# Kernel tuning notes

Measured on AMD Instinct MI355X. Metric: run time of the kernel, lower is better.

The kernel has to match this reference:

```python
import jax, jax.numpy as jnp
import numpy as np

L, B, S, C, H, V = 12, 2, 1024, 768, 12, 50257
D = C // H
FF = 4 * C
SCALE = 1.0 / float(np.sqrt(D))


def setup_inputs() -> dict:
    key = jax.random.key(0)
    ks = jax.random.split(key, 10)
    s = 0.02  # GPT-2 init std
    return {
        "idx": jax.random.randint(ks[0], (B, S), 0, V),
        "targets": jax.random.randint(ks[1], (B, S), 0, V),
        "wte": jax.random.normal(ks[2], (V, C), jnp.float32) * s,
        "wpe": jax.random.normal(ks[3], (S, C), jnp.float32) * s,
        "ln1_w": jnp.ones((L, C), jnp.float32),
        "ln1_b": jnp.zeros((L, C), jnp.float32),
        "qkv_w": jax.random.normal(ks[4], (L, C, 3 * C), jnp.float32) * s,
        "qkv_b": jnp.zeros((L, 3 * C), jnp.float32),
        "proj_w": jax.random.normal(ks[5], (L, C, C), jnp.float32) * s,
        "proj_b": jnp.zeros((L, C), jnp.float32),
        "ln2_w": jnp.ones((L, C), jnp.float32),
        "ln2_b": jnp.zeros((L, C), jnp.float32),
        "fc_w": jax.random.normal(ks[6], (L, C, FF), jnp.float32) * s,
        "fc_b": jnp.zeros((L, FF), jnp.float32),
        "fc2_w": jax.random.normal(ks[7], (L, FF, C), jnp.float32) * s,
        "fc2_b": jnp.zeros((L, C), jnp.float32),
        "lnf_w": jnp.ones((C,), jnp.float32),
        "lnf_b": jnp.zeros((C,), jnp.float32),
    }


def _ln(x, w, b):
    m = jnp.mean(x, axis=-1, keepdims=True)
    v = jnp.mean(jnp.square(x - m), axis=-1, keepdims=True)
    return (x - m) * jax.lax.rsqrt(v + 1e-5) * w + b


def _gpt(wte, wpe, ln1_w, ln1_b, qkv_w, qkv_b, proj_w, proj_b,
         ln2_w, ln2_b, fc_w, fc_b, fc2_w, fc2_b, lnf_w, lnf_b, idx, targets):
    h = wte[idx] + wpe[jnp.arange(S)]  # [B,S,C]
    causal = jnp.tril(jnp.ones((S, S), bool))

    def block(h, p):
        l1w, l1b, qw, qb, pw, pb, l2w, l2b, fw, fb, gw, gb = p
        x = _ln(h, l1w, l1b)
        q, k, v = jnp.split(x @ qw + qb, 3, axis=-1)  # each [B,S,C]
        heads = lambda t: t.reshape(B, S, H, D).transpose(0, 2, 1, 3)  # [B,H,S,D]
        q, k, v = heads(q), heads(k), heads(v)
        scores = jnp.einsum('bhsd,bhtd->bhst', q, k) * SCALE
        scores = jnp.where(causal, scores, -jnp.inf)
        att = jax.nn.softmax(scores, axis=-1)
        o = jnp.einsum('bhst,bhtd->bhsd', att, v)
        o = o.transpose(0, 2, 1, 3).reshape(B, S, C)
        h = h + o @ pw + pb
        x = _ln(h, l2w, l2b)
        h = h + jax.nn.gelu(x @ fw + fb, approximate=True) @ gw + gb
        return h, None

    h, _ = jax.lax.scan(block, h, (ln1_w, ln1_b, qkv_w, qkv_b, proj_w, proj_b,
                                   ln2_w, ln2_b, fc_w, fc_b, fc2_w, fc2_b))
    logits = _ln(h, lnf_w, lnf_b) @ wte.T  # tied lm_head, [B,S,V]
    logp = jax.nn.log_softmax(logits, axis=-1)
    loss = -jnp.mean(jnp.take_along_axis(logp, targets[..., None], axis=-1))
    return logits, loss


def reference(idx, targets, wte, wpe, ln1_w, ln1_b, qkv_w, qkv_b, proj_w, proj_b,
              ln2_w, ln2_b, fc_w, fc_b, fc2_w, fc2_b, lnf_w, lnf_b):
    return _gpt(wte, wpe, ln1_w, ln1_b, qkv_w, qkv_b, proj_w, proj_b,
                ln2_w, ln2_b, fc_w, fc_b, fc2_w, fc2_b, lnf_w, lnf_b, idx, targets)
```

## Files before the change

### kernel.cpp

```cpp
#include <hip/hip_runtime.h>
#include <hip/hip_bf16.h>
#include <cstdint>
#include <cstddef>

constexpr int LNUM = 12;
constexpr int BB   = 2;
constexpr int SS   = 1024;
constexpr int CC   = 768;
constexpr int HH   = 12;
constexpr int DD   = 64;
constexpr int FFD  = 3072;
constexpr int VV   = 50257;
constexpr int VPAD = 50304;
constexpr int MM   = BB * SS;
constexpr int NBX  = VPAD / 128;

typedef unsigned short u16;
typedef short     s16x8 __attribute__((ext_vector_type(8)));
typedef float     f32x4 __attribute__((ext_vector_type(4)));
typedef u16       u16x4 __attribute__((ext_vector_type(4)));
typedef u16       u16x8 __attribute__((ext_vector_type(8)));

__device__ __forceinline__ float bf2f(u16 v) {
    return __uint_as_float(((unsigned)v) << 16);
}
__device__ __forceinline__ u16 f2bf(float f) {
    unsigned u = __float_as_uint(f);
    return (u16)((u + 0x7fffu + ((u >> 16) & 1u)) >> 16);
}


__global__ __launch_bounds__(256) void wte_conv_kernel(const float* __restrict__ wte,
                                                       u16* __restrict__ out) {
    size_t i4 = ((size_t)blockIdx.x * 256 + threadIdx.x) * 4;
    if (i4 >= (size_t)VPAD * CC) return;
    size_t r = i4 / CC;
    u16x4 o;
    if (r < (size_t)VV) {
        const float4 v = *(const float4*)&wte[i4];
        o[0] = f2bf(v.x); o[1] = f2bf(v.y); o[2] = f2bf(v.z); o[3] = f2bf(v.w);
    } else {
        o[0] = o[1] = o[2] = o[3] = 0;
    }
    *(u16x4*)&out[i4] = o;
}

__global__ __launch_bounds__(256) void transpose_conv_kernel(const float* __restrict__ in,
                                                             u16* __restrict__ out,
                                                             int R, int Cn) {
    __shared__ float tile[32][33];
    const float* inp = in + (size_t)blockIdx.z * R * Cn;
    u16* outp = out + (size_t)blockIdx.z * R * Cn;
    int c  = blockIdx.x * 32 + threadIdx.x;
    int r0 = blockIdx.y * 32;
#pragma unroll
    for (int i = 0; i < 4; ++i) {
        int r = r0 + threadIdx.y + i * 8;
        tile[threadIdx.y + i * 8][threadIdx.x] = inp[(size_t)r * Cn + c];
    }
    __syncthreads();
    int oc = r0 + threadIdx.x;
#pragma unroll
    for (int i = 0; i < 4; ++i) {
        int orow = blockIdx.x * 32 + threadIdx.y + i * 8;
        outp[(size_t)orow * R + oc] = f2bf(tile[threadIdx.x][threadIdx.y + i * 8]);
    }
}

__global__ __launch_bounds__(256) void embed_kernel(const int* __restrict__ idx,
                                                    const float* __restrict__ wte,
                                                    const float* __restrict__ wpe,
                                                    float* __restrict__ h) {
    int row = blockIdx.x;
    int s   = row & (SS - 1);
    int tok = idx[row];
    const float* we = wte + (size_t)tok * CC;
    const float* pe = wpe + (size_t)s * CC;
    float* hr = h + (size_t)row * CC;
    for (int c = threadIdx.x; c < CC; c += 256) hr[c] = we[c] + pe[c];
}

__global__ __launch_bounds__(256) void ln_kernel(const float* __restrict__ h,
                                                 const float* __restrict__ w,
                                                 const float* __restrict__ b,
                                                 u16* __restrict__ x) {
    int row = blockIdx.x, tid = threadIdx.x;
    const float* hr = h + (size_t)row * CC;
    float v0 = hr[tid], v1 = hr[tid + 256], v2 = hr[tid + 512];
    float s  = v0 + v1 + v2;
    float s2 = v0 * v0 + v1 * v1 + v2 * v2;
#pragma unroll
    for (int off = 32; off; off >>= 1) {
        s  += __shfl_xor(s, off);
        s2 += __shfl_xor(s2, off);
    }
    __shared__ float rs[4], rs2[4], stat[2];
    int wid = tid >> 6;
    if ((tid & 63) == 0) { rs[wid] = s; rs2[wid] = s2; }
    __syncthreads();
    if (tid == 0) {
        float ts  = rs[0] + rs[1] + rs[2] + rs[3];
        float ts2 = rs2[0] + rs2[1] + rs2[2] + rs2[3];
        float mean = ts * (1.0f / CC);
        float var  = ts2 * (1.0f / CC) - mean * mean;
        stat[0] = mean;
        stat[1] = rsqrtf(var + 1e-5f);
    }
    __syncthreads();
    float mean = stat[0], rstd = stat[1];
    size_t base = (size_t)row * CC;
    x[base + tid]       = f2bf((v0 - mean) * rstd * w[tid]       + b[tid]);
    x[base + tid + 256] = f2bf((v1 - mean) * rstd * w[tid + 256] + b[tid + 256]);
    x[base + tid + 512] = f2bf((v2 - mean) * rstd * w[tid + 512] + b[tid + 512]);
}

template <int BM, int BN, int EPI>
__global__ __launch_bounds__(256)
void gemm_bt_kernel(const u16* __restrict__ A, const u16* __restrict__ Bt,
                    const float* __restrict__ bias, float* __restrict__ outf,
                    u16* __restrict__ outb, int K, long long ldo,
                    float* __restrict__ partM, float* __restrict__ partS) {
    constexpr int MR  = BM / 32, NR = BN / 32;
    constexpr int ACH = BM * 64 / (256 * 8);
    constexpr int BCH = BN * 64 / (256 * 8);
    __shared__ u16 As[BM * 64];
    __shared__ u16 Bs[BN * 64];
    const int tid  = threadIdx.x;
    const int lane = tid & 63;
    const int wid  = tid >> 6;
    const int l15  = lane & 15;
    const int lq   = lane >> 4;
    const int wm   = wid & 1;
    const int wn   = wid >> 1;
    const int rx   = l15 & 7;

    const int gx = gridDim.x, gy = gridDim.y;
    const int nwg = gx * gy;
    const int pos = blockIdx.y * gx + blockIdx.x;
    const int qc  = nwg >> 3, rc = nwg & 7;
    const int xcd = pos & 7, cidx = pos >> 3;
    const int wgid = (xcd < rc ? xcd * (qc + 1) : rc * (qc + 1) + (xcd - rc) * qc) + cidx;
    const int bx = wgid / gy, by = wgid % gy;
    const int bm0 = by * BM, bn0 = bx * BN;

    f32x4 acc[MR][NR];
#pragma unroll
    for (int m = 0; m < MR; ++m)
#pragma unroll
        for (int n = 0; n < NR; ++n) acc[m][n] = (f32x4){0.f, 0.f, 0.f, 0.f};

    u16x8 areg[ACH], breg[BCH];
    auto ldreg = [&](int kt) {
#pragma unroll
        for (int it = 0; it < ACH; ++it) {
            int g = it * 256 + tid, r = g >> 3, c = ((g & 7) ^ (r & 7)) * 8;
            areg[it] = *(const u16x8*)&A[(size_t)(bm0 + r) * (size_t)K + kt + c];
        }
#pragma unroll
        for (int it = 0; it < BCH; ++it) {
            int g = it * 256 + tid, r = g >> 3, c = ((g & 7) ^ (r & 7)) * 8;
            breg[it] = *(const u16x8*)&Bt[(size_t)(bn0 + r) * (size_t)K + kt + c];
        }
    };
    auto wlds = [&]() {
#pragma unroll
        for (int it = 0; it < ACH; ++it) *(u16x8*)&As[(it * 256 + tid) * 8] = areg[it];
#pragma unroll
        for (int it = 0; it < BCH; ++it) *(u16x8*)&Bs[(it * 256 + tid) * 8] = breg[it];
    };
    auto compute = [&]() {
#pragma unroll
        for (int ks = 0; ks < 2; ++ks) {
            s16x8 af[MR], bfr[NR];
#pragma unroll
            for (int m = 0; m < MR; ++m) {
                int row = wm * (BM / 2) + m * 16 + l15;
                af[m] = *(const s16x8*)&As[row * 64 + (((ks * 4 + lq) ^ rx) * 8)];
            }
#pragma unroll
            for (int n = 0; n < NR; ++n) {
                int row = wn * (BN / 2) + n * 16 + l15;
                bfr[n] = *(const s16x8*)&Bs[row * 64 + (((ks * 4 + lq) ^ rx) * 8)];
            }
#pragma unroll
            for (int m = 0; m < MR; ++m)
#pragma unroll
                for (int n = 0; n < NR; ++n)
                    acc[m][n] = __builtin_amdgcn_mfma_f32_16x16x32_bf16(af[m], bfr[n], acc[m][n], 0, 0, 0);
        }
    };

    const int nk = K >> 6;
    ldreg(0);
    for (int t = 0; t < nk; ++t) {
        __syncthreads();
        wlds();
        __syncthreads();
        if (t + 1 < nk) ldreg((t + 1) << 6);
        compute();
    }

#pragma unroll
    for (int m = 0; m < MR; ++m) {
#pragma unroll
        for (int n = 0; n < NR; ++n) {
#pragma unroll
            for (int r = 0; r < 4; ++r) {
                int row = bm0 + wm * (BM / 2) + m * 16 + lq * 4 + r;
                int col = bn0 + wn * (BN / 2) + n * 16 + l15;
                float v = acc[m][n][r];
                if (EPI != 3) v += bias[col];
                if (EPI == 1) {
                    float xg = v;
                    v = 0.5f * xg * (1.0f + tanhf(0.7978845608028654f * (xg + 0.044715f * xg * xg * xg)));
                }
                if (EPI == 0 || EPI == 1) {
                    outb[(size_t)row * ldo + col] = f2bf(v);
                } else if (EPI == 2) {
                    outf[(size_t)row * ldo + col] += v;
                } else {
                    if (col < VV) outf[(size_t)row * ldo + col] = v;
                }
            }
        }
    }

    if constexpr (EPI == 3) {
        __shared__ float redM[2][BM], redS[2][BM];
#pragma unroll
        for (int m = 0; m < MR; ++m) {
#pragma unroll
            for (int r = 0; r < 4; ++r) {
                float mx = -3.0e38f;
#pragma unroll
                for (int n = 0; n < NR; ++n) {
                    int colg = bn0 + wn * (BN / 2) + n * 16 + l15;
                    float v = (colg < VV) ? acc[m][n][r] : -3.0e38f;
                    mx = fmaxf(mx, v);
                }
#pragma unroll
                for (int off = 1; off < 16; off <<= 1) mx = fmaxf(mx, __shfl_xor(mx, off));
                float sm = 0.f;
#pragma unroll
                for (int n = 0; n < NR; ++n) {
                    int colg = bn0 + wn * (BN / 2) + n * 16 + l15;
                    if (colg < VV) sm += __expf(acc[m][n][r] - mx);
                }
#pragma unroll
                for (int off = 1; off < 16; off <<= 1) sm += __shfl_xor(sm, off);
                if (l15 == 0) {
                    int rl = wm * (BM / 2) + m * 16 + lq * 4 + r;
                    redM[wn][rl] = mx;
                    redS[wn][rl] = sm;
                }
            }
        }
        __syncthreads();
        if (tid < BM) {
            float m0 = redM[0][tid], m1 = redM[1][tid];
            float M = fmaxf(m0, m1);
            float S = redS[0][tid] * __expf(m0 - M) + redS[1][tid] * __expf(m1 - M);
            size_t rowg = (size_t)(bm0 + tid);
            partM[rowg * NBX + bx] = M;
            partS[rowg * NBX + bx] = S;
        }
    }
}

__global__ __launch_bounds__(256) void vtrans_kernel(const u16* __restrict__ qkv,
                                                     u16* __restrict__ vT) {
    __shared__ u16 T[64 * 64];
    const int tid = threadIdx.x;
    const int t0  = blockIdx.x * 64;
    const int bh  = blockIdx.y;
    const int b   = bh / HH, hh = bh % HH;
    const u16* vp = qkv + (size_t)b * SS * (3 * CC) + 2 * CC + hh * DD;
#pragma unroll
    for (int it = 0; it < 2; ++it) {
        int g = it * 256 + tid;
        int t = g >> 3, dg = g & 7;
        u16x8 v = *(const u16x8*)&vp[(size_t)(t0 + t) * (3 * CC) + dg * 8];
        *(u16x8*)&T[(t * 8 + (dg ^ (t & 7))) * 8] = v;
    }
    __syncthreads();
    u16* op = vT + (size_t)bh * DD * SS + t0;
#pragma unroll
    for (int it = 0; it < 2; ++it) {
        int g = it * 256 + tid;
        int d = g >> 3, tc = g & 7;
        u16x8 o;
#pragma unroll
        for (int e = 0; e < 8; ++e) {
            int t = tc * 8 + e;
            o[e] = T[(t * 8 + ((d >> 3) ^ (t & 7))) * 8 + (d & 7)];
        }
        *(u16x8*)&op[(size_t)d * SS + tc * 8] = o;
    }
}

__global__ __launch_bounds__(256) void attn_mfma2_kernel(const u16* __restrict__ qkv,
                                                         const u16* __restrict__ vT,
                                                         u16* __restrict__ o) {
    constexpr int PADC = 72;
    __shared__ u16 Ks[64][PADC];
    __shared__ u16 Vs[64][PADC];
    __shared__ u16 Ps[4][2][16][PADC];

    const int tid = threadIdx.x, lane = tid & 63, wid = tid >> 6;
    const int l15 = lane & 15, lq = lane >> 4;
    const int pos = blockIdx.x;
    const int bh  = (pos & 7) + 8 * ((pos >> 3) >> 3);
    const int jlo = (pos >> 3) & 7;
    const int jhi = 15 - jlo;
    const int b   = bh / HH, hh = bh % HH;
    const int q0lo = jlo * 64, q0hi = jhi * 64;

    const size_t base = (size_t)b * SS * (3 * CC);
    const u16* kp = qkv + base + CC + hh * DD;
    const u16* vp = vT + (size_t)bh * DD * SS;

    s16x8 qA[2], qB[2];
    {
        const u16* qr = qkv + base + hh * DD + (size_t)(q0hi + wid * 16 + l15) * (3 * CC);
        qA[0] = *(const s16x8*)&qr[lq * 8];
        qA[1] = *(const s16x8*)&qr[32 + lq * 8];
        const u16* qr2 = qkv + base + hh * DD + (size_t)(q0lo + wid * 16 + l15) * (3 * CC);
        qB[0] = *(const s16x8*)&qr2[lq * 8];
        qB[1] = *(const s16x8*)&qr2[32 + lq * 8];
    }

    float mA[4], lA[4], mB[4], lB[4];
    f32x4 oA[4], oB[4];
#pragma unroll
    for (int r = 0; r < 4; ++r) { mA[r] = mB[r] = -3.0e38f; lA[r] = lB[r] = 0.f; }
#pragma unroll
    for (int nd = 0; nd < 4; ++nd) { oA[nd] = (f32x4){0.f,0.f,0.f,0.f}; oB[nd] = (f32x4){0.f,0.f,0.f,0.f}; }

    auto smax = [&](f32x4 (&sc)[4], float (&m)[4], float (&lsum)[4], f32x4 (&acc)[4],
                    int ptile, int rowq0, bool diag, int t0) {
        if (diag) {
#pragma unroll
            for (int n = 0; n < 4; ++n) {
                int colg = t0 + n * 16 + l15;
#pragma unroll
                for (int r = 0; r < 4; ++r) {
                    int rowg = rowq0 + wid * 16 + lq * 4 + r;
                    float sv = sc[n][r] * 0.125f;
                    sc[n][r] = (colg <= rowg) ? sv : -3.0e38f;
                }
            }
        } else {
#pragma unroll
            for (int n = 0; n < 4; ++n)
#pragma unroll
                for (int r = 0; r < 4; ++r) sc[n][r] *= 0.125f;
        }
        float mt[4];
#pragma unroll
        for (int r = 0; r < 4; ++r)
            mt[r] = fmaxf(fmaxf(sc[0][r], sc[1][r]), fmaxf(sc[2][r], sc[3][r]));
#pragma unroll
        for (int off = 1; off < 16; off <<= 1)
#pragma unroll
            for (int r = 0; r < 4; ++r) mt[r] = fmaxf(mt[r], __shfl_xor(mt[r], off));
        float rs[4];
#pragma unroll
        for (int r = 0; r < 4; ++r) {
            float mn  = fmaxf(m[r], mt[r]);
            float scl = __expf(m[r] - mn);
            m[r] = mn;
            float ps = 0.f;
#pragma unroll
            for (int n = 0; n < 4; ++n) {
                float p = __expf(sc[n][r] - mn);
                sc[n][r] = p;
                ps += p;
            }
            rs[r] = ps;
            lsum[r] *= scl;
#pragma unroll
            for (int nd = 0; nd < 4; ++nd) acc[nd][r] *= scl;
        }
#pragma unroll
        for (int off = 1; off < 16; off <<= 1)
#pragma unroll
            for (int r = 0; r < 4; ++r) rs[r] += __shfl_xor(rs[r], off);
#pragma unroll
        for (int r = 0; r < 4; ++r) lsum[r] += rs[r];
#pragma unroll
        for (int n = 0; n < 4; ++n)
#pragma unroll
            for (int r = 0; r < 4; ++r)
                Ps[wid][ptile][lq * 4 + r][n * 16 + l15] = f2bf(sc[n][r]);
    };

    for (int tt = 0; tt <= jhi; ++tt) {
        const int t0 = tt * 64;
        const bool dolo = (tt <= jlo);
        __syncthreads();
#pragma unroll
        for (int it = 0; it < 2; ++it) {
            int g = it * 256 + tid;
            int r = g >> 3, c = (g & 7) * 8;
            *(u16x8*)&Ks[r][c] = *(const u16x8*)&kp[(size_t)(t0 + r) * (3 * CC) + c];
            *(u16x8*)&Vs[r][c] = *(const u16x8*)&vp[(size_t)r * SS + t0 + c];
        }
        __syncthreads();

        f32x4 sA[4], sB[4];
#pragma unroll
        for (int n = 0; n < 4; ++n) { sA[n] = (f32x4){0.f,0.f,0.f,0.f}; sB[n] = (f32x4){0.f,0.f,0.f,0.f}; }
#pragma unroll
        for (int ks = 0; ks < 2; ++ks) {
            s16x8 kb[4];
#pragma unroll
            for (int n = 0; n < 4; ++n)
                kb[n] = *(const s16x8*)&Ks[n * 16 + l15][ks * 32 + lq * 8];
#pragma unroll
            for (int n = 0; n < 4; ++n)
                sA[n] = __builtin_amdgcn_mfma_f32_16x16x32_bf16(qA[ks], kb[n], sA[n], 0, 0, 0);
            if (dolo) {
#pragma unroll
                for (int n = 0; n < 4; ++n)
                    sB[n] = __builtin_amdgcn_mfma_f32_16x16x32_bf16(qB[ks], kb[n], sB[n], 0, 0, 0);
            }
        }

        smax(sA, mA, lA, oA, 0, q0hi, tt == jhi, t0);
        if (dolo) smax(sB, mB, lB, oB, 1, q0lo, tt == jlo, t0);

#pragma unroll
        for (int ks = 0; ks < 2; ++ks) {
            s16x8 vb[4];
#pragma unroll
            for (int nd = 0; nd < 4; ++nd)
                vb[nd] = *(const s16x8*)&Vs[nd * 16 + l15][ks * 32 + lq * 8];
            s16x8 paA = *(const s16x8*)&Ps[wid][0][l15][ks * 32 + lq * 8];
#pragma unroll
            for (int nd = 0; nd < 4; ++nd)
                oA[nd] = __builtin_amdgcn_mfma_f32_16x16x32_bf16(paA, vb[nd], oA[nd], 0, 0, 0);
            if (dolo) {
                s16x8 paB = *(const s16x8*)&Ps[wid][1][l15][ks * 32 + lq * 8];
#pragma unroll
                for (int nd = 0; nd < 4; ++nd)
                    oB[nd] = __builtin_amdgcn_mfma_f32_16x16x32_bf16(paB, vb[nd], oB[nd], 0, 0, 0);
            }
        }
    }

    auto writeO = [&](float (&lsum)[4], f32x4 (&acc)[4], int rowq0) {
#pragma unroll
        for (int r = 0; r < 4; ++r) {
            float inv = 1.f / lsum[r];
            int rowg = rowq0 + wid * 16 + lq * 4 + r;
            u16* orow = o + ((size_t)b * SS + rowg) * CC + hh * DD;
#pragma unroll
            for (int nd = 0; nd < 4; ++nd)
                orow[nd * 16 + l15] = f2bf(acc[nd][r] * inv);
        }
    };
    writeO(lA, oA, q0hi);
    writeO(lB, oB, q0lo);
}

__global__ __launch_bounds__(256) void lse_kernel(const float* __restrict__ partM,
                                                  const float* __restrict__ partS,
                                                  const float* __restrict__ logits,
                                                  const int* __restrict__ tgt,
                                                  float* __restrict__ lossp) {
    int row = blockIdx.x, tid = threadIdx.x;
    float m = -3.0e38f, s = 0.f;
    for (int i = tid; i < NBX; i += 256) {
        float pm = partM[(size_t)row * NBX + i];
        float ps = partS[(size_t)row * NBX + i];
        float nm = fmaxf(m, pm);
        s = s * __expf(m - nm) + ps * __expf(pm - nm);
        m = nm;
    }
#pragma unroll
    for (int off = 32; off; off >>= 1) {
        float om = __shfl_xor(m, off), os = __shfl_xor(s, off);
        float nm = fmaxf(m, om);
        s = s * __expf(m - nm) + os * __expf(om - nm);
        m = nm;
    }
    __shared__ float rm[4], rsh[4];
    int wid = tid >> 6;
    if ((tid & 63) == 0) { rm[wid] = m; rsh[wid] = s; }
    __syncthreads();
    if (tid == 0) {
        float M = fmaxf(fmaxf(rm[0], rm[1]), fmaxf(rm[2], rm[3]));
        float S = rsh[0] * __expf(rm[0] - M) + rsh[1] * __expf(rm[1] - M) +
                  rsh[2] * __expf(rm[2] - M) + rsh[3] * __expf(rm[3] - M);
        float lse = M + __logf(S);
        lossp[row] = lse - logits[(size_t)row * VV + tgt[row]];
    }
}

__global__ __launch_bounds__(256) void loss_reduce_kernel(const float* __restrict__ lossp,
                                                          float* __restrict__ out) {
    int tid = threadIdx.x;
    float s = 0.f;
    for (int i = tid; i < MM; i += 256) s += lossp[i];
#pragma unroll
    for (int off = 32; off; off >>= 1) s += __shfl_xor(s, off);
    __shared__ float r[4];
    if ((tid & 63) == 0) r[tid >> 6] = s;
    __syncthreads();
    if (tid == 0) out[0] = (r[0] + r[1] + r[2] + r[3]) * (1.0f / MM);
}

extern "C" void kernel_launch(void* const* d_in, const int* in_sizes, int n_in,
                              void* d_out, int out_size, void* d_ws, size_t ws_size,
                              hipStream_t stream) {
    const int*   idx     = (const int*)  d_in[0];
    const int*   targets = (const int*)  d_in[1];
    const float* wte     = (const float*)d_in[2];
    const float* wpe     = (const float*)d_in[3];
    const float* ln1w    = (const float*)d_in[4];
    const float* ln1b    = (const float*)d_in[5];
    const float* qkvw    = (const float*)d_in[6];
    const float* qkvbi   = (const float*)d_in[7];
    const float* projw   = (const float*)d_in[8];
    const float* projbi  = (const float*)d_in[9];
    const float* ln2w    = (const float*)d_in[10];
    const float* ln2b    = (const float*)d_in[11];
    const float* fcw     = (const float*)d_in[12];
    const float* fcbi    = (const float*)d_in[13];
    const float* fc2w    = (const float*)d_in[14];
    const float* fc2bi   = (const float*)d_in[15];
    const float* lnfw    = (const float*)d_in[16];
    const float* lnfb    = (const float*)d_in[17];
    float* logits = (float*)d_out;

    char* wsb = (char*)d_ws;
    size_t off = 0;
    auto alloc = [&](size_t n) -> char* {
        char* p = wsb + off;
        off = (off + n + 255) & ~(size_t)255;
        return p;
    };
    u16*   wteT  = (u16*)  alloc((size_t)VPAD * CC * 2);
    u16*   qkvT  = (u16*)  alloc((size_t)LNUM * 3 * CC * CC * 2);
    u16*   projT = (u16*)  alloc((size_t)LNUM * CC * CC * 2);
    u16*   fcT   = (u16*)  alloc((size_t)LNUM * FFD * CC * 2);
    u16*   fc2T  = (u16*)  alloc((size_t)LNUM * CC * FFD * 2);
    float* h     = (float*)alloc((size_t)MM * CC * 4);
    u16*   xb    = (u16*)  alloc((size_t)MM * CC * 2);
    u16*   qkvb  = (u16*)  alloc((size_t)MM * 3 * CC * 2);
    u16*   ob    = (u16*)  alloc((size_t)MM * CC * 2);
    u16*   gb    = (u16*)  alloc((size_t)MM * FFD * 2);
    u16*   vTb   = (u16*)  alloc((size_t)BB * HH * DD * SS * 2);
    float* lossp = (float*)alloc((size_t)MM * 4);
    float* partM = (float*)alloc((size_t)MM * NBX * 4);
    float* partS = (float*)alloc((size_t)MM * NBX * 4);

    {
        int blocks = (int)(((size_t)VPAD * CC / 4 + 255) / 256);
        wte_conv_kernel<<<blocks, 256, 0, stream>>>(wte, wteT);
    }
    transpose_conv_kernel<<<dim3(3 * CC / 32, CC / 32, LNUM), dim3(32, 8), 0, stream>>>(qkvw, qkvT, CC, 3 * CC);
    transpose_conv_kernel<<<dim3(CC / 32, CC / 32, LNUM),     dim3(32, 8), 0, stream>>>(projw, projT, CC, CC);
    transpose_conv_kernel<<<dim3(FFD / 32, CC / 32, LNUM),    dim3(32, 8), 0, stream>>>(fcw, fcT, CC, FFD);
    transpose_conv_kernel<<<dim3(CC / 32, FFD / 32, LNUM),    dim3(32, 8), 0, stream>>>(fc2w, fc2T, FFD, CC);

    embed_kernel<<<MM, 256, 0, stream>>>(idx, wte, wpe, h);

    for (int l = 0; l < LNUM; ++l) {
        const u16* qkvT_l  = qkvT  + (size_t)l * 3 * CC * CC;
        const u16* projT_l = projT + (size_t)l * CC * CC;
        const u16* fcT_l   = fcT   + (size_t)l * FFD * CC;
        const u16* fc2T_l  = fc2T  + (size_t)l * CC * FFD;

        ln_kernel<<<MM, 256, 0, stream>>>(h, ln1w + (size_t)l * CC, ln1b + (size_t)l * CC, xb);
        gemm_bt_kernel<128, 128, 0><<<dim3(3 * CC / 128, MM / 128), 256, 0, stream>>>(
            xb, qkvT_l, qkvbi + (size_t)l * 3 * CC, nullptr, qkvb, CC, 3 * CC, nullptr, nullptr);
        vtrans_kernel<<<dim3(SS / 64, BB * HH), 256, 0, stream>>>(qkvb, vTb);
        attn_mfma2_kernel<<<BB * HH * 8, 256, 0, stream>>>(qkvb, vTb, ob);
        gemm_bt_kernel<64, 64, 2><<<dim3(CC / 64, MM / 64), 256, 0, stream>>>(
            ob, projT_l, projbi + (size_t)l * CC, h, nullptr, CC, CC, nullptr, nullptr);
        ln_kernel<<<MM, 256, 0, stream>>>(h, ln2w + (size_t)l * CC, ln2b + (size_t)l * CC, xb);
        gemm_bt_kernel<128, 128, 1><<<dim3(FFD / 128, MM / 128), 256, 0, stream>>>(
            xb, fcT_l, fcbi + (size_t)l * FFD, nullptr, gb, CC, FFD, nullptr, nullptr);
        gemm_bt_kernel<64, 64, 2><<<dim3(CC / 64, MM / 64), 256, 0, stream>>>(
            gb, fc2T_l, fc2bi + (size_t)l * CC, h, nullptr, FFD, CC, nullptr, nullptr);
    }

    ln_kernel<<<MM, 256, 0, stream>>>(h, lnfw, lnfb, xb);
    gemm_bt_kernel<128, 128, 3><<<dim3(VPAD / 128, MM / 128), 256, 0, stream>>>(
        xb, wteT, nullptr, logits, nullptr, CC, VV, partM, partS);

    lse_kernel<<<MM, 256, 0, stream>>>(partM, partS, logits, targets, lossp);
    loss_reduce_kernel<<<1, 256, 0, stream>>>(lossp, logits + (size_t)MM * VV);
}
```

Before: 2.085 ms.

## Fuse LayerNorm into GEMM A-loads and V transpose into QKV epilogue

Removes the per-layer ln_kernel launches. Row sum and sum-of-squares statistics are now accumulated with atomics in the residual-add GEMM epilogues (and in the embedding kernel), and normalization is applied when fp32 h tiles are staged into LDS inside the QKV and FC GEMMs. The V-transpose kernel is also folded into the QKV GEMM epilogue, which writes V directly in transposed layout. The cost is reading fp32 A (twice the bytes) in the LN-fused GEMMs and recomputing normalization per N-tile. A one-pass variance formula and atomics add some numerical and contention risk.

Result: slower. 2.400 ms (+15.1%).

```diff
diff --git a/kernel.cpp b/kernel.cpp
--- a/kernel.cpp
+++ b/kernel.cpp
@@ -70,14 +70,34 @@
 __global__ __launch_bounds__(256) void embed_kernel(const int* __restrict__ idx,
                                                     const float* __restrict__ wte,
                                                     const float* __restrict__ wpe,
-                                                    float* __restrict__ h) {
+                                                    float* __restrict__ h,
+                                                    float* __restrict__ stats0) {
     int row = blockIdx.x;
+    int tid = threadIdx.x;
     int s   = row & (SS - 1);
     int tok = idx[row];
     const float* we = wte + (size_t)tok * CC;
     const float* pe = wpe + (size_t)s * CC;
     float* hr = h + (size_t)row * CC;
-    for (int c = threadIdx.x; c < CC; c += 256) hr[c] = we[c] + pe[c];
+    float sm = 0.f, sq = 0.f;
+    for (int c = tid; c < CC; c += 256) {
+        float v = we[c] + pe[c];
+        hr[c] = v;
+        sm += v; sq += v * v;
+    }
+#pragma unroll
+    for (int off = 32; off; off >>= 1) {
+        sm += __shfl_xor(sm, off);
+        sq += __shfl_xor(sq, off);
+    }
+    __shared__ float rs[4], rs2[4];
+    int wid = tid >> 6;
+    if ((tid & 63) == 0) { rs[wid] = sm; rs2[wid] = sq; }
+    __syncthreads();
+    if (tid == 0) {
+        stats0[row * 2]     = rs[0] + rs[1] + rs[2] + rs[3];
+        stats0[row * 2 + 1] = rs2[0] + rs2[1] + rs2[2] + rs2[3];
+    }
 }
 
 __global__ __launch_bounds__(256) void ln_kernel(const float* __restrict__ h,
@@ -114,11 +134,15 @@
     x[base + tid + 512] = f2bf((v2 - mean) * rstd * w[tid + 512] + b[tid + 512]);
 }
 
-template <int BM, int BN, int EPI>
+template <int BM, int BN, int EPI, bool LNA>
 __global__ __launch_bounds__(256)
-void gemm_bt_kernel(const u16* __restrict__ A, const u16* __restrict__ Bt,
-                    const float* __restrict__ bias, float* __restrict__ outf,
-                    u16* __restrict__ outb, int K, long long ldo,
+void gemm_bt_kernel(const u16* __restrict__ Ab, const float* __restrict__ Af,
+                    const float* __restrict__ Ast,
+                    const float* __restrict__ lnw, const float* __restrict__ lnb,
+                    const u16* __restrict__ Bt, const float* __restrict__ bias,
+                    float* __restrict__ outf, u16* __restrict__ outb,
+                    u16* __restrict__ vT, float* __restrict__ stats_out,
+                    int K, long long ldo,
                     float* __restrict__ partM, float* __restrict__ partS) {
     constexpr int MR  = BM / 32, NR = BN / 32;
     constexpr int ACH = BM * 64 / (256 * 8);
@@ -150,11 +174,20 @@
         for (int n = 0; n < NR; ++n) acc[m][n] = (f32x4){0.f, 0.f, 0.f, 0.f};
 
     u16x8 areg[ACH], breg[BCH];
+    float fareg[LNA ? ACH : 1][8];
     auto ldreg = [&](int kt) {
 #pragma unroll
         for (int it = 0; it < ACH; ++it) {
             int g = it * 256 + tid, r = g >> 3, c = ((g & 7) ^ (r & 7)) * 8;
-            areg[it] = *(const u16x8*)&A[(size_t)(bm0 + r) * (size_t)K + kt + c];
+            if constexpr (LNA) {
+                const float* hp = &Af[(size_t)(bm0 + r) * (size_t)K + kt + c];
+                float4 h0 = *(const float4*)hp;
+                float4 h1 = *(const float4*)(hp + 4);
+                fareg[it][0] = h0.x; fareg[it][1] = h0.y; fareg[it][2] = h0.z; fareg[it][3] = h0.w;
+                fareg[it][4] = h1.x; fareg[it][5] = h1.y; fareg[it][6] = h1.z; fareg[it][7] = h1.w;
+            } else {
+                areg[it] = *(const u16x8*)&Ab[(size_t)(bm0 + r) * (size_t)K + kt + c];
+            }
         }
 #pragma unroll
         for (int it = 0; it < BCH; ++it) {
@@ -162,9 +195,32 @@
             breg[it] = *(const u16x8*)&Bt[(size_t)(bn0 + r) * (size_t)K + kt + c];
         }
     };
-    auto wlds = [&]() {
-#pragma unroll
-        for (int it = 0; it < ACH; ++it) *(u16x8*)&As[(it * 256 + tid) * 8] = areg[it];
+    auto wlds = [&](int kt) {
+#pragma unroll
+        for (int it = 0; it < ACH; ++it) {
+            if constexpr (LNA) {
+                int g = it * 256 + tid, r = g >> 3, c = ((g & 7) ^ (r & 7)) * 8;
+                float sum = Ast[(bm0 + r) * 2], ssq = Ast[(bm0 + r) * 2 + 1];
+                float mean = sum * (1.0f / CC);
+                float rstd = rsqrtf(ssq * (1.0f / CC) - mean * mean + 1e-5f);
+                const float* wp = &lnw[kt + c];
+                const float* bp = &lnb[kt + c];
+                float4 w0 = *(const float4*)wp, w1 = *(const float4*)(wp + 4);
+                float4 b0 = *(const float4*)bp, b1 = *(const float4*)(bp + 4);
+                u16x8 pk;
+                pk[0] = f2bf((fareg[it][0] - mean) * rstd * w0.x + b0.x);
+                pk[1] = f2bf((fareg[it][1] - mean) * rstd * w0.y + b0.y);
+                pk[2] = f2bf((fareg[it][2] - mean) * rstd * w0.z + b0.z);
+                pk[3] = f2bf((fareg[it][3] - mean) * rstd * w0.w + b0.w);
+                pk[4] = f2bf((fareg[it][4] - mean) * rstd * w1.x + b1.x);
+                pk[5] = f2bf((fareg[it][5] - mean) * rstd * w1.y + b1.y);
+                pk[6] = f2bf((fareg[it][6] - mean) * rstd * w1.z + b1.z);
+                pk[7] = f2bf((fareg[it][7] - mean) * rstd * w1.w + b1.w);
+                *(u16x8*)&As[(it * 256 + tid) * 8] = pk;
+            } else {
+                *(u16x8*)&As[(it * 256 + tid) * 8] = areg[it];
+            }
+        }
 #pragma unroll
         for (int it = 0; it < BCH; ++it) *(u16x8*)&Bs[(it * 256 + tid) * 8] = breg[it];
     };
@@ -194,20 +250,32 @@
     ldreg(0);
     for (int t = 0; t < nk; ++t) {
         __syncthreads();
-        wlds();
+        wlds(t << 6);
         __syncthreads();
         if (t + 1 < nk) ldreg((t + 1) << 6);
         compute();
     }
 
+    float hv[EPI == 2 ? MR : 1][EPI == 2 ? NR : 1][4];
 #pragma unroll
     for (int m = 0; m < MR; ++m) {
 #pragma unroll
         for (int n = 0; n < NR; ++n) {
+            int col = bn0 + wn * (BN / 2) + n * 16 + l15;
+            if (EPI == 0 && col >= 2 * CC) {
+                int hd = col - 2 * CC;
+                int hh2 = hd >> 6, d = hd & 63;
+                int rowg0 = bm0 + wm * (BM / 2) + m * 16 + lq * 4;
+                int b2 = rowg0 >> 10, s0 = rowg0 & (SS - 1);
+                u16x4 o4;
+#pragma unroll
+                for (int r = 0; r < 4; ++r) o4[r] = f2bf(acc[m][n][r] + bias[col]);
+                *(u16x4*)&vT[(((size_t)(b2 * HH + hh2)) * DD + d) * SS + s0] = o4;
+                continue;
+            }
 #pragma unroll
             for (int r = 0; r < 4; ++r) {
                 int row = bm0 + wm * (BM / 2) + m * 16 + lq * 4 + r;
-                int col = bn0 + wn * (BN / 2) + n * 16 + l15;
                 float v = acc[m][n][r];
                 if (EPI != 3) v += bias[col];
                 if (EPI == 1) {
@@ -217,9 +285,33 @@
                 if (EPI == 0 || EPI == 1) {
                     outb[(size_t)row * ldo + col] = f2bf(v);
                 } else if (EPI == 2) {
-                    outf[(size_t)row * ldo + col] += v;
+                    float nh = outf[(size_t)row * ldo + col] + v;
+                    outf[(size_t)row * ldo + col] = nh;
+                    hv[m][n][r] = nh;
                 } else {
                     if (col < VV) outf[(size_t)row * ldo + col] = v;
+                }
+            }
+        }
+    }
+
+    if constexpr (EPI == 2) {
+#pragma unroll
+        for (int m = 0; m < MR; ++m) {
+#pragma unroll
+            for (int r = 0; r < 4; ++r) {
+                float p = 0.f, p2 = 0.f;
+#pragma unroll
+                for (int n = 0; n < NR; ++n) { p += hv[m][n][r]; p2 += hv[m][n][r] * hv[m][n][r]; }
+#pragma unroll
+                for (int off = 1; off < 16; off <<= 1) {
+                    p  += __shfl_xor(p, off);
+                    p2 += __shfl_xor(p2, off);
+                }
+                if (l15 == 0) {
+                    int row = bm0 + wm * (BM / 2) + m * 16 + lq * 4 + r;
+                    atomicAdd(&stats_out[row * 2], p);
+                    atomicAdd(&stats_out[row * 2 + 1], p2);
                 }
             }
         }
@@ -264,37 +356,6 @@
             partM[rowg * NBX + bx] = M;
             partS[rowg * NBX + bx] = S;
         }
-    }
-}
-
-__global__ __launch_bounds__(256) void vtrans_kernel(const u16* __restrict__ qkv,
-                                                     u16* __restrict__ vT) {
-    __shared__ u16 T[64 * 64];
-    const int tid = threadIdx.x;
-    const int t0  = blockIdx.x * 64;
-    const int bh  = blockIdx.y;
-    const int b   = bh / HH, hh = bh % HH;
-    const u16* vp = qkv + (size_t)b * SS * (3 * CC) + 2 * CC + hh * DD;
-#pragma unroll
-    for (int it = 0; it < 2; ++it) {
-        int g = it * 256 + tid;
-        int t = g >> 3, dg = g & 7;
-        u16x8 v = *(const u16x8*)&vp[(size_t)(t0 + t) * (3 * CC) + dg * 8];
-        *(u16x8*)&T[(t * 8 + (dg ^ (t & 7))) * 8] = v;
-    }
-    __syncthreads();
-    u16* op = vT + (size_t)bh * DD * SS + t0;
-#pragma unroll
-    for (int it = 0; it < 2; ++it) {
-        int g = it * 256 + tid;
-        int d = g >> 3, tc = g & 7;
-        u16x8 o;
-#pragma unroll
-        for (int e = 0; e < 8; ++e) {
-            int t = tc * 8 + e;
-            o[e] = T[(t * 8 + ((d >> 3) ^ (t & 7))) * 8 + (d & 7)];
-        }
-        *(u16x8*)&op[(size_t)d * SS + tc * 8] = o;
     }
 }
 
@@ -554,6 +615,10 @@
     float* lossp = (float*)alloc((size_t)MM * 4);
     float* partM = (float*)alloc((size_t)MM * NBX * 4);
     float* partS = (float*)alloc((size_t)MM * NBX * 4);
+    float* ln1st = (float*)alloc((size_t)(LNUM + 1) * MM * 2 * 4);
+    float* ln2st = (float*)alloc((size_t)LNUM * MM * 2 * 4);
+
+    hipMemsetAsync(ln1st, 0, (size_t)(2 * LNUM + 1) * MM * 2 * 4, stream);
 
     {
         int blocks = (int)(((size_t)VPAD * CC / 4 + 255) / 256);
@@ -564,31 +629,41 @@
     transpose_conv_kernel<<<dim3(FFD / 32, CC / 32, LNUM),    dim3(32, 8), 0, stream>>>(fcw, fcT, CC, FFD);
     transpose_conv_kernel<<<dim3(CC / 32, FFD / 32, LNUM),    dim3(32, 8), 0, stream>>>(fc2w, fc2T, FFD, CC);
 
-    embed_kernel<<<MM, 256, 0, stream>>>(idx, wte, wpe, h);
+    embed_kernel<<<MM, 256, 0, stream>>>(idx, wte, wpe, h, ln1st);
 
     for (int l = 0; l < LNUM; ++l) {
         const u16* qkvT_l  = qkvT  + (size_t)l * 3 * CC * CC;
         const u16* projT_l = projT + (size_t)l * CC * CC;
         const u16* fcT_l   = fcT   + (size_t)l * FFD * CC;
         const u16* fc2T_l  = fc2T  + (size_t)l * CC * FFD;
-
-        ln_kernel<<<MM, 256, 0, stream>>>(h, ln1w + (size_t)l * CC, ln1b + (size_t)l * CC, xb);
-        gemm_bt_kernel<128, 128, 0><<<dim3(3 * CC / 128, MM / 128), 256, 0, stream>>>(
-            xb, qkvT_l, qkvbi + (size_t)l * 3 * CC, nullptr, qkvb, CC, 3 * CC, nullptr, nullptr);
-        vtrans_kernel<<<dim3(SS / 64, BB * HH), 256, 0, stream>>>(qkvb, vTb);
+        float* ln1st_l = ln1st + (size_t)l * MM * 2;
+        float* ln2st_l = ln2st + (size_t)l * MM * 2;
+
+        gemm_bt_kernel<128, 128, 0, true><<<dim3(3 * CC / 128, MM / 128), 256, 0, stream>>>(
+            nullptr, h, ln1st_l, ln1w + (size_t)l * CC, ln1b + (size_t)l * CC,
+            qkvT_l, qkvbi + (size_t)l * 3 * CC, nullptr, qkvb, vTb, nullptr,
+            CC, 3 * CC, nullptr, nullptr);
         attn_mfma2_kernel<<<BB * HH * 8, 256, 0, stream>>>(qkvb, vTb, ob);
-        gemm_bt_kernel<64, 64, 2><<<dim3(CC / 64, MM / 64), 256, 0, stream>>>(
-            ob, projT_l, projbi + (size_t)l * CC, h, nullptr, CC, CC, nullptr, nullptr);
-        ln_kernel<<<MM, 256, 0, stream>>>(h, ln2w + (size_t)l * CC, ln2b + (size_t)l * CC, xb);
-        gemm_bt_kernel<128, 128, 1><<<dim3(FFD / 128, MM / 128), 256, 0, stream>>>(
-            xb, fcT_l, fcbi + (size_t)l * FFD, nullptr, gb, CC, FFD, nullptr, nullptr);
-        gemm_bt_kernel<64, 64, 2><<<dim3(CC / 64, MM / 64), 256, 0, stream>>>(
-            gb, fc2T_l, fc2bi + (size_t)l * CC, h, nullptr, FFD, CC, nullptr, nullptr);
+        gemm_bt_kernel<64, 64, 2, false><<<dim3(CC / 64, MM / 64), 256, 0, stream>>>(
+            ob, nullptr, nullptr, nullptr, nullptr,
+            projT_l, projbi + (size_t)l * CC, h, nullptr, nullptr, ln2st_l,
+            CC, CC, nullptr, nullptr);
+        gemm_bt_kernel<128, 128, 1, true><<<dim3(FFD / 128, MM / 128), 256, 0, stream>>>(
+            nullptr, h, ln2st_l, ln2w + (size_t)l * CC, ln2b + (size_t)l * CC,
+            fcT_l, fcbi + (size_t)l * FFD, nullptr, gb, nullptr, nullptr,
+            CC, FFD, nullptr, nullptr);
+        gemm_bt_kernel<64, 64, 2, false><<<dim3(CC / 64, MM / 64), 256, 0, stream>>>(
+            gb, nullptr, nullptr, nullptr, nullptr,
+            fc2T_l, fc2bi + (size_t)l * CC, h, nullptr, nullptr,
+            ln1st + (size_t)(l + 1) * MM * 2,
+            FFD, CC, nullptr, nullptr);
     }
 
     ln_kernel<<<MM, 256, 0, stream>>>(h, lnfw, lnfb, xb);
-    gemm_bt_kernel<128, 128, 3><<<dim3(VPAD / 128, MM / 128), 256, 0, stream>>>(
-        xb, wteT, nullptr, logits, nullptr, CC, VV, partM, partS);
+    gemm_bt_kernel<128, 128, 3, false><<<dim3(VPAD / 128, MM / 128), 256, 0, stream>>>(
+        xb, nullptr, nullptr, nullptr, nullptr,
+        wteT, nullptr, logits, nullptr, nullptr, nullptr,
+        CC, VV, partM, partS);
 
     lse_kernel<<<MM, 256, 0, stream>>>(partM, partS, logits, targets, lossp);
     loss_reduce_kernel<<<1, 256, 0, stream>>>(lossp, logits + (size_t)MM * VV);
```
